# Kernel tuning notes

Hardware: AMD Instinct MI355X
Metric: run time of the kernel (lower is better)

## Reference

```python
import jax, jax.numpy as jnp
import numpy as np

EPS = 1e-5  # BatchNorm1d default eps


def setup_inputs() -> dict:
    key = jax.random.key(0)
    k1, k2 = jax.random.split(key)
    b, d, h, w = 32, 256, 32, 128
    x = jax.random.normal(k1, (b, d, h, w), dtype=jnp.float32)
    # mask=True means padded/masked position (excluded from stats, left untouched)
    mask = jax.random.randint(k2, (b, 1, h, w), 0, 2).astype(bool)
    gamma = jnp.ones((d,), dtype=jnp.float32)
    beta = jnp.zeros((d,), dtype=jnp.float32)
    return {"x": x, "mask": mask, "gamma": gamma, "beta": beta}


def reference(x, mask, gamma, beta):
    # x: [b, d, h, w], mask: [b, 1, h, w] (True = masked)
    not_mask = ~mask[:, 0]                      # [b, h, w]
    wgt = not_mask.astype(x.dtype)              # [b, h, w]
    count = jnp.maximum(wgt.sum(), jnp.asarray(1.0, x.dtype))
    xt = jnp.transpose(x, (0, 2, 3, 1))         # [b, h, w, d]
    wm = wgt[..., None]                         # [b, h, w, 1]
    # masked per-channel batch statistics (biased variance, as BN training mode)
    mean = (xt * wm).sum(axis=(0, 1, 2)) / count                  # [d]
    var = (wm * (xt - mean) ** 2).sum(axis=(0, 1, 2)) / count     # [d]
    normed = (xt - mean) * jax.lax.rsqrt(var + EPS) * gamma + beta
    out = jnp.where(not_mask[..., None], normed, xt)              # scatter-back
    return jnp.transpose(out, (0, 3, 1, 2))     # [b, d, h, w]
```

## Files before the change

### kernel.cpp

```cpp
#include <hip/hip_runtime.h>

#define BB 32
#define DD 256
#define HW 4096
#define DHW (DD * HW)
#define TOTAL (BB * DHW)
#define NSLICE (BB * DD)
#define EPS 1e-5f

typedef float floatx4 __attribute__((ext_vector_type(4)));


__global__ void __launch_bounds__(256)
stats_kernel(const float* __restrict__ x, const int* __restrict__ mask,
             float* __restrict__ ws) {
    const int slice = blockIdx.x;
    const int b = slice >> 8;
    const int d = slice & 255;
    const float4* xs = reinterpret_cast<const float4*>(
        x + (size_t)b * DHW + (size_t)d * HW);
    const int4* ms = reinterpret_cast<const int4*>(mask + b * HW);
    const int tid = threadIdx.x;

    float sum = 0.f, sq = 0.f, cnt = 0.f;
#pragma unroll
    for (int j = 0; j < 4; ++j) {
        const int v = j * 256 + tid;
        float4 xv = xs[v];
        int4 mv = ms[v];
        if (!mv.x) { sum += xv.x; sq += xv.x * xv.x; cnt += 1.f; }
        if (!mv.y) { sum += xv.y; sq += xv.y * xv.y; cnt += 1.f; }
        if (!mv.z) { sum += xv.z; sq += xv.z * xv.z; cnt += 1.f; }
        if (!mv.w) { sum += xv.w; sq += xv.w * xv.w; cnt += 1.f; }
    }

#pragma unroll
    for (int off = 32; off > 0; off >>= 1) {
        sum += __shfl_down(sum, off);
        sq  += __shfl_down(sq, off);
        cnt += __shfl_down(cnt, off);
    }

    __shared__ float ssum[4], ssq[4], scnt[4];
    const int wave = tid >> 6, lane = tid & 63;
    if (lane == 0) { ssum[wave] = sum; ssq[wave] = sq; scnt[wave] = cnt; }
    __syncthreads();
    if (tid == 0) {
        float ts = 0.f, tq = 0.f, tc = 0.f;
#pragma unroll
        for (int i = 0; i < 4; ++i) { ts += ssum[i]; tq += ssq[i]; tc += scnt[i]; }
        ws[slice] = ts;
        ws[NSLICE + slice] = tq;
        if (d == 0) ws[2 * NSLICE + b] = tc;
    }
}

__global__ void __launch_bounds__(256)
apply_kernel(const float* __restrict__ x, const int* __restrict__ mask,
             const float* __restrict__ ws, const float* __restrict__ gamma,
             const float* __restrict__ beta, float* __restrict__ out) {
    __shared__ float s_scale[DD], s_bias[DD];
    const int tid = threadIdx.x;

    float cnt = 0.f;
#pragma unroll
    for (int b = 0; b < BB; ++b) cnt += ws[2 * NSLICE + b];
    cnt = fmaxf(cnt, 1.0f);
    float sum = 0.f, sq = 0.f;
#pragma unroll
    for (int b = 0; b < BB; ++b) {
        sum += ws[b * DD + tid];
        sq  += ws[NSLICE + b * DD + tid];
    }
    const float mean = sum / cnt;
    const float var = fmaxf(sq / cnt - mean * mean, 0.0f);
    const float sc = rsqrtf(var + EPS) * gamma[tid];
    s_scale[tid] = sc;
    s_bias[tid] = beta[tid] - mean * sc;
    __syncthreads();

    const int nvec = TOTAL / 4;
    const int stride = gridDim.x * blockDim.x;
    floatx4* __restrict__ ov = reinterpret_cast<floatx4*>(out);
    for (int v = blockIdx.x * blockDim.x + tid; v < nvec; v += stride) {
        const int e = v << 2;
        const int b = e >> 20;
        const int rem = e & (DHW - 1);
        const int d = rem >> 12;
        const int pos = rem & 4095;
        float4 xv = reinterpret_cast<const float4*>(x)[v];
        int4 mv = reinterpret_cast<const int4*>(mask)[(b * HW + pos) >> 2];
        const float s = s_scale[d], bi = s_bias[d];
        floatx4 o;
        o.x = mv.x ? xv.x : xv.x * s + bi;
        o.y = mv.y ? xv.y : xv.y * s + bi;
        o.z = mv.z ? xv.z : xv.z * s + bi;
        o.w = mv.w ? xv.w : xv.w * s + bi;
        __builtin_nontemporal_store(o, &ov[v]);
    }
}

extern "C" void kernel_launch(void* const* d_in, const int* in_sizes, int n_in,
                              void* d_out, int out_size, void* d_ws, size_t ws_size,
                              hipStream_t stream) {
    const float* x     = (const float*)d_in[0];
    const int*   mask  = (const int*)d_in[1];
    const float* gamma = (const float*)d_in[2];
    const float* beta  = (const float*)d_in[3];
    float* out = (float*)d_out;
    float* ws  = (float*)d_ws;

    stats_kernel<<<NSLICE, 256, 0, stream>>>(x, mask, ws);
    apply_kernel<<<2048, 256, 0, stream>>>(x, mask, ws, gamma, beta, out);
}
```

Measured before the change: 70.00 us.

## Fuse stats and apply passes into one cooperative kernel with grid sync

Replaces the two-kernel stats/apply pipeline with a single cooperative kernel of 512 blocks, each owning 16 consecutive channel slices of one batch. Each block computes its partial sums, writes them to the workspace and waits at a grid-wide sync. It then reduces the per-channel statistics and re-reads its slices in reverse order to normalize, so the second read can hit in cache. This removes a kernel launch and most of the second DRAM pass over x, at the cost of a grid barrier and of requiring all blocks to be co-resident; the old two-kernel path is kept as a fallback.

```diff
diff --git a/kernel.cpp b/kernel.cpp
--- a/kernel.cpp
+++ b/kernel.cpp
@@ -1,15 +1,123 @@
 #include <hip/hip_runtime.h>
+#include <hip/hip_cooperative_groups.h>
+
+namespace cg = cooperative_groups;
 
 #define BB 32
 #define DD 256
 #define HW 4096
-#define DHW (DD * HW)
-#define TOTAL (BB * DHW)
 #define NSLICE (BB * DD)
 #define EPS 1e-5f
 
+#define CNBLK 512
+#define CSPB (NSLICE / CNBLK)
+
 typedef float floatx4 __attribute__((ext_vector_type(4)));
 
+
+__global__ void __launch_bounds__(256, 4)
+fused_kernel(const float* __restrict__ x, const int* __restrict__ mask,
+             const float* __restrict__ gamma, const float* __restrict__ beta,
+             float* __restrict__ ws, float* __restrict__ out) {
+    const int blk = blockIdx.x;
+    const int tid = threadIdx.x;
+    const int wave = tid >> 6, lane = tid & 63;
+    const int slice0 = blk * CSPB;
+    const int b = slice0 >> 8;
+    const int d0 = slice0 & 255;
+
+    __shared__ float ssum[CSPB][4], ssq[CSPB][4], scnt[4];
+    __shared__ float s_scale[CSPB], s_bias[CSPB];
+
+    const int4* ms = reinterpret_cast<const int4*>(mask + b * HW);
+    int4 mreg[4];
+#pragma unroll
+    for (int j = 0; j < 4; ++j) mreg[j] = ms[j * 256 + tid];
+
+    float cnt = 0.f;
+#pragma unroll
+    for (int j = 0; j < 4; ++j) {
+        cnt += (mreg[j].x ? 0.f : 1.f) + (mreg[j].y ? 0.f : 1.f)
+             + (mreg[j].z ? 0.f : 1.f) + (mreg[j].w ? 0.f : 1.f);
+    }
+#pragma unroll
+    for (int off = 32; off > 0; off >>= 1) cnt += __shfl_down(cnt, off);
+    if (lane == 0) scnt[wave] = cnt;
+
+    const float4* xb = reinterpret_cast<const float4*>(x + (size_t)slice0 * HW);
+#pragma unroll
+    for (int s = 0; s < CSPB; ++s) {
+        float sum = 0.f, sq = 0.f;
+#pragma unroll
+        for (int j = 0; j < 4; ++j) {
+            float4 xv = xb[s * 1024 + j * 256 + tid];
+            int4 mv = mreg[j];
+            if (!mv.x) { sum += xv.x; sq += xv.x * xv.x; }
+            if (!mv.y) { sum += xv.y; sq += xv.y * xv.y; }
+            if (!mv.z) { sum += xv.z; sq += xv.z * xv.z; }
+            if (!mv.w) { sum += xv.w; sq += xv.w * xv.w; }
+        }
+#pragma unroll
+        for (int off = 32; off > 0; off >>= 1) {
+            sum += __shfl_down(sum, off);
+            sq  += __shfl_down(sq, off);
+        }
+        if (lane == 0) { ssum[s][wave] = sum; ssq[s][wave] = sq; }
+    }
+    __syncthreads();
+    if (tid < CSPB) {
+        float ts = 0.f, tq = 0.f;
+#pragma unroll
+        for (int w = 0; w < 4; ++w) { ts += ssum[tid][w]; tq += ssq[tid][w]; }
+        ws[slice0 + tid] = ts;
+        ws[NSLICE + slice0 + tid] = tq;
+    }
+    if (tid == 0 && d0 == 0) {
+        ws[2 * NSLICE + b] = scnt[0] + scnt[1] + scnt[2] + scnt[3];
+    }
+    __threadfence();
+    cg::this_grid().sync();
+
+    {
+        const int c = tid >> 4;
+        const int l = tid & 15;
+        float ps = ws[l * DD + d0 + c]          + ws[(l + 16) * DD + d0 + c];
+        float pq = ws[NSLICE + l * DD + d0 + c] + ws[NSLICE + (l + 16) * DD + d0 + c];
+        float pc = ws[2 * NSLICE + l]           + ws[2 * NSLICE + l + 16];
+#pragma unroll
+        for (int off = 8; off > 0; off >>= 1) {
+            ps += __shfl_down(ps, off, 16);
+            pq += __shfl_down(pq, off, 16);
+            pc += __shfl_down(pc, off, 16);
+        }
+        if (l == 0) {
+            pc = fmaxf(pc, 1.0f);
+            const float mean = ps / pc;
+            const float var = fmaxf(pq / pc - mean * mean, 0.0f);
+            const float sc = rsqrtf(var + EPS) * gamma[d0 + c];
+            s_scale[c] = sc;
+            s_bias[c] = beta[d0 + c] - mean * sc;
+        }
+    }
+    __syncthreads();
+
+    floatx4* ob = reinterpret_cast<floatx4*>(out + (size_t)slice0 * HW);
+#pragma unroll
+    for (int s = CSPB - 1; s >= 0; --s) {
+        const float sc = s_scale[s], bi = s_bias[s];
+#pragma unroll
+        for (int j = 0; j < 4; ++j) {
+            float4 xv = xb[s * 1024 + j * 256 + tid];
+            int4 mv = mreg[j];
+            floatx4 o;
+            o.x = mv.x ? xv.x : xv.x * sc + bi;
+            o.y = mv.y ? xv.y : xv.y * sc + bi;
+            o.z = mv.z ? xv.z : xv.z * sc + bi;
+            o.w = mv.w ? xv.w : xv.w * sc + bi;
+            __builtin_nontemporal_store(o, &ob[s * 1024 + j * 256 + tid]);
+        }
+    }
+}
 
 __global__ void __launch_bounds__(256)
 stats_kernel(const float* __restrict__ x, const int* __restrict__ mask,
@@ -18,7 +126,7 @@
     const int b = slice >> 8;
     const int d = slice & 255;
     const float4* xs = reinterpret_cast<const float4*>(
-        x + (size_t)b * DHW + (size_t)d * HW);
+        x + (size_t)b * (DD * HW) + (size_t)d * HW);
     const int4* ms = reinterpret_cast<const int4*>(mask + b * HW);
     const int tid = threadIdx.x;
 
@@ -33,22 +141,20 @@
         if (!mv.z) { sum += xv.z; sq += xv.z * xv.z; cnt += 1.f; }
         if (!mv.w) { sum += xv.w; sq += xv.w * xv.w; cnt += 1.f; }
     }
-
 #pragma unroll
     for (int off = 32; off > 0; off >>= 1) {
         sum += __shfl_down(sum, off);
         sq  += __shfl_down(sq, off);
         cnt += __shfl_down(cnt, off);
     }
-
-    __shared__ float ssum[4], ssq[4], scnt[4];
+    __shared__ float fsum[4], fsq[4], fcnt[4];
     const int wave = tid >> 6, lane = tid & 63;
-    if (lane == 0) { ssum[wave] = sum; ssq[wave] = sq; scnt[wave] = cnt; }
+    if (lane == 0) { fsum[wave] = sum; fsq[wave] = sq; fcnt[wave] = cnt; }
     __syncthreads();
     if (tid == 0) {
         float ts = 0.f, tq = 0.f, tc = 0.f;
 #pragma unroll
-        for (int i = 0; i < 4; ++i) { ts += ssum[i]; tq += ssq[i]; tc += scnt[i]; }
+        for (int i = 0; i < 4; ++i) { ts += fsum[i]; tq += fsq[i]; tc += fcnt[i]; }
         ws[slice] = ts;
         ws[NSLICE + slice] = tq;
         if (d == 0) ws[2 * NSLICE + b] = tc;
@@ -79,17 +185,17 @@
     s_bias[tid] = beta[tid] - mean * sc;
     __syncthreads();
 
-    const int nvec = TOTAL / 4;
+    const int nvec = (BB * DD * HW) / 4;
     const int stride = gridDim.x * blockDim.x;
     floatx4* __restrict__ ov = reinterpret_cast<floatx4*>(out);
     for (int v = blockIdx.x * blockDim.x + tid; v < nvec; v += stride) {
         const int e = v << 2;
-        const int b = e >> 20;
-        const int rem = e & (DHW - 1);
+        const int bidx = e >> 20;
+        const int rem = e & (DD * HW - 1);
         const int d = rem >> 12;
         const int pos = rem & 4095;
         float4 xv = reinterpret_cast<const float4*>(x)[v];
-        int4 mv = reinterpret_cast<const int4*>(mask)[(b * HW + pos) >> 2];
+        int4 mv = reinterpret_cast<const int4*>(mask)[(bidx * HW + pos) >> 2];
         const float s = s_scale[d], bi = s_bias[d];
         floatx4 o;
         o.x = mv.x ? xv.x : xv.x * s + bi;
@@ -110,6 +216,13 @@
     float* out = (float*)d_out;
     float* ws  = (float*)d_ws;
 
-    stats_kernel<<<NSLICE, 256, 0, stream>>>(x, mask, ws);
-    apply_kernel<<<2048, 256, 0, stream>>>(x, mask, ws, gamma, beta, out);
-}
+    void* args[] = {(void*)&x, (void*)&mask, (void*)&gamma, (void*)&beta,
+                    (void*)&ws, (void*)&out};
+    hipError_t err = hipLaunchCooperativeKernel((const void*)fused_kernel,
+                                                dim3(CNBLK), dim3(256),
+                                                args, 0, stream);
+    if (err != hipSuccess) {
+        stats_kernel<<<NSLICE, 256, 0, stream>>>(x, mask, ws);
+        apply_kernel<<<2048, 256, 0, stream>>>(x, mask, ws, gamma, beta, out);
+    }
+}
```

New measurement: 168.4 us. 141% more time.

## Split stats finalize into its own kernel and reverse apply block order

Applied to the files above, without the earlier changes.

Moves the per-channel mean/var/scale computation out of every apply block into a single finalize kernel that writes scale and bias to workspace, so each of the 2048 apply blocks loads only 512 floats instead of re-reducing 64 partial sums per thread. The apply kernel now gives each block a fixed contiguous chunk with a fully unrolled loop and walks chunks in reverse order, so the data most recently read by the stats pass (likely still in the last-level cache) is processed first. This costs one extra small kernel launch.

```diff
diff --git a/kernel.cpp b/kernel.cpp
--- a/kernel.cpp
+++ b/kernel.cpp
@@ -4,12 +4,17 @@
 #define DD 256
 #define HW 4096
 #define DHW (DD * HW)
+#define NSLICE (BB * DD)
 #define TOTAL (BB * DHW)
-#define NSLICE (BB * DD)
 #define EPS 1e-5f
 
+#define WS_SUM   0
+#define WS_SQ    NSLICE
+#define WS_CNT   (2 * NSLICE)
+#define WS_SCALE (2 * NSLICE + 64)
+#define WS_BIAS  (2 * NSLICE + 64 + DD)
+
 typedef float floatx4 __attribute__((ext_vector_type(4)));
-
 
 __global__ void __launch_bounds__(256)
 stats_kernel(const float* __restrict__ x, const int* __restrict__ mask,
@@ -33,63 +38,69 @@
         if (!mv.z) { sum += xv.z; sq += xv.z * xv.z; cnt += 1.f; }
         if (!mv.w) { sum += xv.w; sq += xv.w * xv.w; cnt += 1.f; }
     }
-
 #pragma unroll
     for (int off = 32; off > 0; off >>= 1) {
         sum += __shfl_down(sum, off);
         sq  += __shfl_down(sq, off);
         cnt += __shfl_down(cnt, off);
     }
-
-    __shared__ float ssum[4], ssq[4], scnt[4];
+    __shared__ float fsum[4], fsq[4], fcnt[4];
     const int wave = tid >> 6, lane = tid & 63;
-    if (lane == 0) { ssum[wave] = sum; ssq[wave] = sq; scnt[wave] = cnt; }
+    if (lane == 0) { fsum[wave] = sum; fsq[wave] = sq; fcnt[wave] = cnt; }
     __syncthreads();
     if (tid == 0) {
         float ts = 0.f, tq = 0.f, tc = 0.f;
 #pragma unroll
-        for (int i = 0; i < 4; ++i) { ts += ssum[i]; tq += ssq[i]; tc += scnt[i]; }
-        ws[slice] = ts;
-        ws[NSLICE + slice] = tq;
-        if (d == 0) ws[2 * NSLICE + b] = tc;
+        for (int i = 0; i < 4; ++i) { ts += fsum[i]; tq += fsq[i]; tc += fcnt[i]; }
+        ws[WS_SUM + slice] = ts;
+        ws[WS_SQ + slice] = tq;
+        if (d == 0) ws[WS_CNT + b] = tc;
     }
 }
 
 __global__ void __launch_bounds__(256)
-apply_kernel(const float* __restrict__ x, const int* __restrict__ mask,
-             const float* __restrict__ ws, const float* __restrict__ gamma,
-             const float* __restrict__ beta, float* __restrict__ out) {
-    __shared__ float s_scale[DD], s_bias[DD];
-    const int tid = threadIdx.x;
-
+finalize_kernel(const float* __restrict__ gamma, const float* __restrict__ beta,
+                float* __restrict__ ws) {
+    const int d = threadIdx.x;
     float cnt = 0.f;
 #pragma unroll
-    for (int b = 0; b < BB; ++b) cnt += ws[2 * NSLICE + b];
+    for (int b = 0; b < BB; ++b) cnt += ws[WS_CNT + b];
     cnt = fmaxf(cnt, 1.0f);
     float sum = 0.f, sq = 0.f;
 #pragma unroll
     for (int b = 0; b < BB; ++b) {
-        sum += ws[b * DD + tid];
-        sq  += ws[NSLICE + b * DD + tid];
+        sum += ws[WS_SUM + b * DD + d];
+        sq  += ws[WS_SQ + b * DD + d];
     }
     const float mean = sum / cnt;
     const float var = fmaxf(sq / cnt - mean * mean, 0.0f);
-    const float sc = rsqrtf(var + EPS) * gamma[tid];
-    s_scale[tid] = sc;
-    s_bias[tid] = beta[tid] - mean * sc;
+    const float sc = rsqrtf(var + EPS) * gamma[d];
+    ws[WS_SCALE + d] = sc;
+    ws[WS_BIAS + d] = beta[d] - mean * sc;
+}
+
+__global__ void __launch_bounds__(256)
+apply_kernel(const float* __restrict__ x, const int* __restrict__ mask,
+             const float* __restrict__ ws, float* __restrict__ out) {
+    __shared__ float s_scale[DD], s_bias[DD];
+    const int tid = threadIdx.x;
+    s_scale[tid] = ws[WS_SCALE + tid];
+    s_bias[tid] = ws[WS_BIAS + tid];
     __syncthreads();
 
-    const int nvec = TOTAL / 4;
-    const int stride = gridDim.x * blockDim.x;
+    const int chunk = (gridDim.x - 1) - blockIdx.x;
+    const int cb = chunk * 4096;
     floatx4* __restrict__ ov = reinterpret_cast<floatx4*>(out);
-    for (int v = blockIdx.x * blockDim.x + tid; v < nvec; v += stride) {
+#pragma unroll
+    for (int j = 0; j < 16; ++j) {
+        const int v = cb + j * 256 + tid;
         const int e = v << 2;
-        const int b = e >> 20;
+        const int bidx = e >> 20;
         const int rem = e & (DHW - 1);
         const int d = rem >> 12;
         const int pos = rem & 4095;
         float4 xv = reinterpret_cast<const float4*>(x)[v];
-        int4 mv = reinterpret_cast<const int4*>(mask)[(b * HW + pos) >> 2];
+        int4 mv = reinterpret_cast<const int4*>(mask)[(bidx * HW + pos) >> 2];
         const float s = s_scale[d], bi = s_bias[d];
         floatx4 o;
         o.x = mv.x ? xv.x : xv.x * s + bi;
@@ -111,5 +122,6 @@
     float* ws  = (float*)d_ws;
 
     stats_kernel<<<NSLICE, 256, 0, stream>>>(x, mask, ws);
-    apply_kernel<<<2048, 256, 0, stream>>>(x, mask, ws, gamma, beta, out);
+    finalize_kernel<<<1, 256, 0, stream>>>(gamma, beta, ws);
+    apply_kernel<<<2048, 256, 0, stream>>>(x, mask, ws, out);
 }
```

Result: no change. 69.21 us (-1.1%).

## Fuse stats and apply into one persistent kernel with grid-wide barrier

Applied to the files above, without the earlier changes.

Replaces the two-kernel stats/apply pipeline with a single persistent kernel of 256 blocks of 1024 threads. Each block handles 32 slices, computes their partial statistics, waits at a global atomic-counter barrier, then normalizes the same slices. The goal is to remove the second kernel launch and to re-read x mostly from cache (MI355X has a large last-level cache) instead of fetching all of it from DRAM a second time. It adds a memset launch and a spin barrier, which depends on all 256 blocks being resident at once, so there is a deadlock risk if occupancy falls short.

```diff
diff --git a/kernel.cpp b/kernel.cpp
--- a/kernel.cpp
+++ b/kernel.cpp
@@ -4,99 +4,128 @@
 #define DD 256
 #define HW 4096
 #define DHW (DD * HW)
-#define TOTAL (BB * DHW)
 #define NSLICE (BB * DD)
 #define EPS 1e-5f
 
+#define FNBLK 256
+#define FSPB (NSLICE / FNBLK)
+
+#define WS_SUM 0
+#define WS_SQ  NSLICE
+#define WS_CNT (2 * NSLICE)
+#define WS_CTR (2 * NSLICE + 64)
+
 typedef float floatx4 __attribute__((ext_vector_type(4)));
 
+__global__ void __launch_bounds__(1024)
+fused2_kernel(const float* __restrict__ x, const int* __restrict__ mask,
+              const float* __restrict__ gamma, const float* __restrict__ beta,
+              float* __restrict__ ws, float* __restrict__ out) {
+    const int blk = blockIdx.x;
+    const int tid = threadIdx.x;
+    const int wave = tid >> 6, lane = tid & 63;
+    const int slice0 = blk * FSPB;
+    const int b = slice0 >> 8;
+    const int d0 = slice0 & 255;
 
-__global__ void __launch_bounds__(256)
-stats_kernel(const float* __restrict__ x, const int* __restrict__ mask,
-             float* __restrict__ ws) {
-    const int slice = blockIdx.x;
-    const int b = slice >> 8;
-    const int d = slice & 255;
-    const float4* xs = reinterpret_cast<const float4*>(
-        x + (size_t)b * DHW + (size_t)d * HW);
-    const int4* ms = reinterpret_cast<const int4*>(mask + b * HW);
-    const int tid = threadIdx.x;
+    __shared__ float ssum[FSPB][16], ssq[FSPB][16], scnt[16];
+    __shared__ float s_scale[FSPB], s_bias[FSPB];
 
-    float sum = 0.f, sq = 0.f, cnt = 0.f;
+    const int4 mv = reinterpret_cast<const int4*>(mask + b * HW)[tid];
+
+    {
+        float c = (mv.x ? 0.f : 1.f) + (mv.y ? 0.f : 1.f)
+                + (mv.z ? 0.f : 1.f) + (mv.w ? 0.f : 1.f);
 #pragma unroll
-    for (int j = 0; j < 4; ++j) {
-        const int v = j * 256 + tid;
-        float4 xv = xs[v];
-        int4 mv = ms[v];
-        if (!mv.x) { sum += xv.x; sq += xv.x * xv.x; cnt += 1.f; }
-        if (!mv.y) { sum += xv.y; sq += xv.y * xv.y; cnt += 1.f; }
-        if (!mv.z) { sum += xv.z; sq += xv.z * xv.z; cnt += 1.f; }
-        if (!mv.w) { sum += xv.w; sq += xv.w * xv.w; cnt += 1.f; }
+        for (int off = 32; off > 0; off >>= 1) c += __shfl_down(c, off);
+        if (lane == 0) scnt[wave] = c;
     }
 
+    const float4* xb = reinterpret_cast<const float4*>(x + (size_t)slice0 * HW);
 #pragma unroll
-    for (int off = 32; off > 0; off >>= 1) {
-        sum += __shfl_down(sum, off);
-        sq  += __shfl_down(sq, off);
-        cnt += __shfl_down(cnt, off);
+    for (int s = 0; s < FSPB; ++s) {
+        float4 xv = xb[s * 1024 + tid];
+        float sum = 0.f, sq = 0.f;
+        if (!mv.x) { sum += xv.x; sq += xv.x * xv.x; }
+        if (!mv.y) { sum += xv.y; sq += xv.y * xv.y; }
+        if (!mv.z) { sum += xv.z; sq += xv.z * xv.z; }
+        if (!mv.w) { sum += xv.w; sq += xv.w * xv.w; }
+#pragma unroll
+        for (int off = 32; off > 0; off >>= 1) {
+            sum += __shfl_down(sum, off);
+            sq  += __shfl_down(sq, off);
+        }
+        if (lane == 0) { ssum[s][wave] = sum; ssq[s][wave] = sq; }
     }
-
-    __shared__ float ssum[4], ssq[4], scnt[4];
-    const int wave = tid >> 6, lane = tid & 63;
-    if (lane == 0) { ssum[wave] = sum; ssq[wave] = sq; scnt[wave] = cnt; }
     __syncthreads();
-    if (tid == 0) {
-        float ts = 0.f, tq = 0.f, tc = 0.f;
+    if (tid < 512) {
+        const int s = tid >> 4, w = tid & 15;
+        float ts = ssum[s][w], tq = ssq[s][w];
 #pragma unroll
-        for (int i = 0; i < 4; ++i) { ts += ssum[i]; tq += ssq[i]; tc += scnt[i]; }
-        ws[slice] = ts;
-        ws[NSLICE + slice] = tq;
-        if (d == 0) ws[2 * NSLICE + b] = tc;
+        for (int off = 8; off > 0; off >>= 1) {
+            ts += __shfl_down(ts, off, 16);
+            tq += __shfl_down(tq, off, 16);
+        }
+        if (w == 0) {
+            ws[WS_SUM + slice0 + s] = ts;
+            ws[WS_SQ + slice0 + s] = tq;
+        }
     }
-}
-
-__global__ void __launch_bounds__(256)
-apply_kernel(const float* __restrict__ x, const int* __restrict__ mask,
-             const float* __restrict__ ws, const float* __restrict__ gamma,
-             const float* __restrict__ beta, float* __restrict__ out) {
-    __shared__ float s_scale[DD], s_bias[DD];
-    const int tid = threadIdx.x;
-
-    float cnt = 0.f;
+    if (tid == 0 && d0 == 0) {
+        float tc = 0.f;
 #pragma unroll
-    for (int b = 0; b < BB; ++b) cnt += ws[2 * NSLICE + b];
-    cnt = fmaxf(cnt, 1.0f);
-    float sum = 0.f, sq = 0.f;
-#pragma unroll
-    for (int b = 0; b < BB; ++b) {
-        sum += ws[b * DD + tid];
-        sq  += ws[NSLICE + b * DD + tid];
+        for (int i = 0; i < 16; ++i) tc += scnt[i];
+        ws[WS_CNT + b] = tc;
     }
-    const float mean = sum / cnt;
-    const float var = fmaxf(sq / cnt - mean * mean, 0.0f);
-    const float sc = rsqrtf(var + EPS) * gamma[tid];
-    s_scale[tid] = sc;
-    s_bias[tid] = beta[tid] - mean * sc;
     __syncthreads();
 
-    const int nvec = TOTAL / 4;
-    const int stride = gridDim.x * blockDim.x;
-    floatx4* __restrict__ ov = reinterpret_cast<floatx4*>(out);
-    for (int v = blockIdx.x * blockDim.x + tid; v < nvec; v += stride) {
-        const int e = v << 2;
-        const int b = e >> 20;
-        const int rem = e & (DHW - 1);
-        const int d = rem >> 12;
-        const int pos = rem & 4095;
-        float4 xv = reinterpret_cast<const float4*>(x)[v];
-        int4 mv = reinterpret_cast<const int4*>(mask)[(b * HW + pos) >> 2];
-        const float s = s_scale[d], bi = s_bias[d];
+    unsigned* ctr = reinterpret_cast<unsigned*>(ws + WS_CTR);
+    if (tid == 0) {
+        __hip_atomic_fetch_add(ctr, 1u, __ATOMIC_RELEASE, __HIP_MEMORY_SCOPE_AGENT);
+        while (__hip_atomic_load(ctr, __ATOMIC_ACQUIRE, __HIP_MEMORY_SCOPE_AGENT)
+               < (unsigned)FNBLK) {
+            __builtin_amdgcn_s_sleep(2);
+        }
+    }
+    __syncthreads();
+
+    {
+        const int g = tid >> 5, bl = tid & 31;
+        const int ch = d0 + g;
+        float ps = __hip_atomic_load(&ws[WS_SUM + bl * DD + ch],
+                                     __ATOMIC_RELAXED, __HIP_MEMORY_SCOPE_AGENT);
+        float pq = __hip_atomic_load(&ws[WS_SQ + bl * DD + ch],
+                                     __ATOMIC_RELAXED, __HIP_MEMORY_SCOPE_AGENT);
+        float pc = __hip_atomic_load(&ws[WS_CNT + bl],
+                                     __ATOMIC_RELAXED, __HIP_MEMORY_SCOPE_AGENT);
+#pragma unroll
+        for (int off = 16; off > 0; off >>= 1) {
+            ps += __shfl_down(ps, off, 32);
+            pq += __shfl_down(pq, off, 32);
+            pc += __shfl_down(pc, off, 32);
+        }
+        if (bl == 0) {
+            pc = fmaxf(pc, 1.0f);
+            const float mean = ps / pc;
+            const float var = fmaxf(pq / pc - mean * mean, 0.0f);
+            const float sc = rsqrtf(var + EPS) * gamma[ch];
+            s_scale[g] = sc;
+            s_bias[g] = beta[ch] - mean * sc;
+        }
+    }
+    __syncthreads();
+
+    floatx4* ob = reinterpret_cast<floatx4*>(out + (size_t)slice0 * HW);
+#pragma unroll
+    for (int s = 0; s < FSPB; ++s) {
+        const float sc = s_scale[s], bi = s_bias[s];
+        float4 xv = xb[s * 1024 + tid];
         floatx4 o;
-        o.x = mv.x ? xv.x : xv.x * s + bi;
-        o.y = mv.y ? xv.y : xv.y * s + bi;
-        o.z = mv.z ? xv.z : xv.z * s + bi;
-        o.w = mv.w ? xv.w : xv.w * s + bi;
-        __builtin_nontemporal_store(o, &ov[v]);
+        o.x = mv.x ? xv.x : xv.x * sc + bi;
+        o.y = mv.y ? xv.y : xv.y * sc + bi;
+        o.z = mv.z ? xv.z : xv.z * sc + bi;
+        o.w = mv.w ? xv.w : xv.w * sc + bi;
+        __builtin_nontemporal_store(o, &ob[s * 1024 + tid]);
     }
 }
 
@@ -110,6 +139,6 @@
     float* out = (float*)d_out;
     float* ws  = (float*)d_ws;
 
-    stats_kernel<<<NSLICE, 256, 0, stream>>>(x, mask, ws);
-    apply_kernel<<<2048, 256, 0, stream>>>(x, mask, ws, gamma, beta, out);
+    hipMemsetAsync((char*)d_ws + WS_CTR * sizeof(float), 0, sizeof(unsigned), stream);
+    fused2_kernel<<<FNBLK, 1024, 0, stream>>>(x, mask, gamma, beta, ws, out);
 }
```

New measurement: 104.8 us. 1.5x slower.
